# Performance work log

Measured on AMD Instinct MI355X. Metric: run time of the kernel, lower is better.

The kernel has to match this reference:

```python
import jax, jax.numpy as jnp
import numpy as np

B, S, H = 1, 2048, 2048
NH = 16            # num attention heads
QLR = 1536         # q_lora_rank
KVLR = 512         # kv_lora_rank
DR = 64            # qk_rope_head_dim
DN = 128           # qk_nope_head_dim
DV = 128           # v_head_dim
DQK = DN + DR      # qk_head_dim = 192
EPS = 1e-6


def rmsnorm(x, w):
    xf = x.astype(jnp.float32)
    var = jnp.mean(xf * xf, axis=-1, keepdims=True)
    return (xf * jax.lax.rsqrt(var + EPS)).astype(x.dtype) * w


def rotate_half(x):
    d = x.shape[-1] // 2
    return jnp.concatenate([-x[..., d:], x[..., :d]], axis=-1)


def rope_interleave(x, cos, sin):
    # x: [b, h, s, d]; de-interleave pairs (even dims -> first half, odd -> second)
    b, h, s, d = x.shape
    x = x.reshape(b, h, s, d // 2, 2).swapaxes(-1, -2).reshape(b, h, s, d)
    return x * cos + rotate_half(x) * sin


def setup_inputs() -> dict:
    key = jax.random.key(0)
    ks = jax.random.split(key, 8)
    std = 0.02
    hidden_states = jax.random.normal(ks[0], (B, S, H), jnp.float32)
    # real rotary cos/sin for a 64-dim rope slice
    pos = jnp.arange(S, dtype=jnp.float32)
    inv_freq = 1.0 / (10000.0 ** (jnp.arange(0, DR, 2, dtype=jnp.float32) / DR))
    ang = pos[:, None] * inv_freq[None, :]            # [S, DR//2]
    emb = jnp.concatenate([ang, ang], axis=-1)        # [S, DR]
    cos = jnp.broadcast_to(jnp.cos(emb)[None], (B, S, DR)).astype(jnp.float32)
    sin = jnp.broadcast_to(jnp.sin(emb)[None], (B, S, DR)).astype(jnp.float32)
    # weights stored [in, out]
    wq_a = jax.random.normal(ks[1], (H, QLR), jnp.float32) * std
    q_ln = jnp.ones((QLR,), jnp.float32)
    wq_b = jax.random.normal(ks[2], (QLR, NH * DQK), jnp.float32) * std
    wkv_a = jax.random.normal(ks[3], (H, KVLR + DR), jnp.float32) * std
    kv_ln = jnp.ones((KVLR,), jnp.float32)
    wkv_b = jax.random.normal(ks[4], (KVLR, NH * (DN + DV)), jnp.float32) * std
    wo = jax.random.normal(ks[5], (NH * DV, H), jnp.float32) * std
    return {"hidden_states": hidden_states, "cos": cos, "sin": sin,
            "wq_a": wq_a, "q_ln": q_ln, "wq_b": wq_b,
            "wkv_a": wkv_a, "kv_ln": kv_ln, "wkv_b": wkv_b, "wo": wo}


def reference(hidden_states, cos, sin, wq_a, q_ln, wq_b, wkv_a, kv_ln, wkv_b, wo):
    b, s, _ = hidden_states.shape
    # low-rank Q: a-proj -> RMSNorm -> b-proj
    q = rmsnorm(hidden_states @ wq_a, q_ln) @ wq_b           # [b, s, NH*DQK]
    q = q.reshape(b, s, NH, DQK).transpose(0, 2, 1, 3)       # [b, NH, s, DQK]
    q_pass, q_rot = q[..., :DN], q[..., DN:]
    # compressed KV with shared rope key
    ckv = hidden_states @ wkv_a                               # [b, s, KVLR+DR]
    kv_c, k_rot = ckv[..., :KVLR], ckv[..., KVLR:]
    kv = (rmsnorm(kv_c, kv_ln) @ wkv_b).reshape(b, s, NH, DN + DV).transpose(0, 2, 1, 3)
    k_pass, v = kv[..., :DN], kv[..., DN:]
    k_rot = k_rot[:, None, :, :]                              # [b, 1, s, DR]
    cos4, sin4 = cos[:, None], sin[:, None]
    q_rot = rope_interleave(q_rot, cos4, sin4)
    k_rot = rope_interleave(k_rot, cos4, sin4)
    k_rot = jnp.broadcast_to(k_rot, (b, NH, s, DR))
    qs = jnp.concatenate([q_pass, q_rot], axis=-1)            # [b, NH, s, DQK]
    ks_ = jnp.concatenate([k_pass, k_rot], axis=-1)
    scaling = DQK ** -0.5
    scores = jnp.einsum('bhqd,bhkd->bhqk', qs, ks_) * scaling
    causal = jnp.tril(jnp.ones((s, s), bool))
    scores = jnp.where(causal, scores, jnp.finfo(scores.dtype).min)
    probs = jax.nn.softmax(scores.astype(jnp.float32), axis=-1).astype(qs.dtype)
    out = jnp.einsum('bhqk,bhkd->bhqd', probs, v)             # [b, NH, s, DV]
    out = out.transpose(0, 2, 1, 3).reshape(b, s, NH * DV)
    return out @ wo
```

## Files before the change

kernel.cpp:

```cpp
#include <hip/hip_runtime.h>
#include <hip/hip_bf16.h>
#include <stdint.h>

#define S_    2048
#define H_    2048
#define NH_   16
#define QLR_  1536
#define KVLR_ 512
#define DR_   64
#define DN_   128
#define DV_   128
#define DQK_  192
#define QW_   (NH_*DQK_)
#define KVW_  (NH_*(DN_+DV_))
#define CKVW_ (KVLR_+DR_)

typedef __attribute__((ext_vector_type(8))) short short8;
typedef __attribute__((ext_vector_type(4))) float floatx4;

__device__ __forceinline__ unsigned short f2bf(float f) {
    unsigned u = __float_as_uint(f);
    unsigned r = u + 0x7fffu + ((u >> 16) & 1u);
    return (unsigned short)(r >> 16);
}
__device__ __forceinline__ float bf2f(unsigned short h) {
    return __uint_as_float(((unsigned)h) << 16);
}
__device__ __forceinline__ void store_out(float* p, float v) { *p = v; }
__device__ __forceinline__ void store_out(unsigned short* p, float v) { *p = f2bf(v); }

typedef const __attribute__((address_space(1))) unsigned int* gas_ptr;
typedef __attribute__((address_space(3))) unsigned int* las_ptr;
__device__ __forceinline__ void gload16(const void* g, void* l) {
    __builtin_amdgcn_global_load_lds((gas_ptr)g, (las_ptr)l, 16, 0, 0);
}

__device__ __forceinline__ int xcd_swz(int orig, int nwg) {
    int q8 = nwg >> 3, r8 = nwg & 7;
    int xcd = orig & 7, jj = orig >> 3;
    return (xcd < r8 ? xcd * (q8 + 1) : r8 * (q8 + 1) + (xcd - r8) * q8) + jj;
}

#define GEMM_STAGE(b, k0) do {                                               \
        _Pragma("unroll")                                                    \
        for (int sub = 0; sub < 2; ++sub) {                                  \
            int m = tid >> 2, k8 = tid & 3;                                  \
            gload16(A + (size_t)(bm + m) * lda + (k0) + sub * 32 + k8 * 8,   \
                    &As[b][sub][tid * 8]);                                   \
        }                                                                    \
        _Pragma("unroll")                                                    \
        for (int sub = 0; sub < 2; ++sub)                                    \
            _Pragma("unroll")                                                \
            for (int j = 0; j < 2; ++j) {                                    \
                int ch = j * 256 + tid;                                      \
                int n = ch >> 2, k8 = ch & 3;                                \
                int nrow = bn + n; if (nrow >= N) nrow = N - 1;              \
                gload16(Bt + (size_t)nrow * K + (k0) + sub * 32 + k8 * 8,    \
                        &Bs[b][sub][ch * 8]);                                \
            }                                                                \
    } while (0)

#define GEMM_COMPUTE_SUB(sub) do {                                           \
        short8 a[2], b[4];                                                   \
        _Pragma("unroll")                                                    \
        for (int mi = 0; mi < 2; ++mi)                                       \
            a[mi] = *(const short8*)&As[cur][sub][(wm + mi * 16 + cc) * 32 + g * 8]; \
        _Pragma("unroll")                                                    \
        for (int ni = 0; ni < 4; ++ni)                                       \
            b[ni] = *(const short8*)&Bs[cur][sub][(wn + ni * 16 + cc) * 32 + g * 8]; \
        __builtin_amdgcn_s_setprio(1);                                       \
        _Pragma("unroll")                                                    \
        for (int mi = 0; mi < 2; ++mi)                                       \
            _Pragma("unroll")                                                \
            for (int ni = 0; ni < 4; ++ni)                                   \
                acc[mi][ni] = __builtin_amdgcn_mfma_f32_16x16x32_bf16(       \
                    a[mi], b[ni], acc[mi][ni], 0, 0, 0);                     \
        __builtin_amdgcn_s_setprio(0);                                       \
    } while (0)

template <typename OutT>
__global__ __launch_bounds__(256) void gemm_bf16_db(
    const unsigned short* __restrict__ A, const unsigned short* __restrict__ Bt,
    OutT* __restrict__ C, int M, int N, int K, int lda, int ldc)
{
    __shared__ unsigned short As[2][2][64 * 32];
    __shared__ unsigned short Bs[2][2][128 * 32];

    const int tid = threadIdx.x;
    const int l = tid & 63;
    const int g = l >> 4, cc = l & 15;
    const int w = tid >> 6;
    const int wm = (w >> 1) * 32, wn = (w & 1) * 64;

    const int nwg = gridDim.x * gridDim.y;
    const int wg = xcd_swz(blockIdx.y * gridDim.x + blockIdx.x, nwg);
    const int bm = (wg / gridDim.x) * 64;
    const int bn = (wg % gridDim.x) * 128;

    floatx4 acc[2][4];
#pragma unroll
    for (int i = 0; i < 2; i++)
#pragma unroll
        for (int j = 0; j < 4; j++) acc[i][j] = (floatx4){0.f, 0.f, 0.f, 0.f};

    GEMM_STAGE(0, 0);
    __syncthreads();
    int cur = 0;

    for (int k0 = 0; k0 < K; k0 += 64) {
        if (k0 + 64 < K) GEMM_STAGE(cur ^ 1, k0 + 64);
        GEMM_COMPUTE_SUB(0);
        GEMM_COMPUTE_SUB(1);
        __syncthreads();
        cur ^= 1;
    }

#pragma unroll
    for (int mi = 0; mi < 2; ++mi)
#pragma unroll
        for (int ni = 0; ni < 4; ++ni)
#pragma unroll
            for (int i = 0; i < 4; ++i) {
                int row = bm + wm + mi * 16 + g * 4 + i;
                int col = bn + wn + ni * 16 + cc;
                if (col < N) store_out(&C[(size_t)row * ldc + col], acc[mi][ni][i]);
            }
}

__global__ __launch_bounds__(256) void gemm_bf16_dual(
    const unsigned short* __restrict__ A, const unsigned short* __restrict__ Bt,
    float* __restrict__ C0, float* __restrict__ C1,
    int M, int N, int K, int lda, int ldc0, int ldc1)
{
    __shared__ unsigned short As[2][2][64 * 32];
    __shared__ unsigned short Bs[2][2][128 * 32];

    const int tid = threadIdx.x;
    const int l = tid & 63;
    const int g = l >> 4, cc = l & 15;
    const int w = tid >> 6;
    const int wm = (w >> 1) * 32, wn = (w & 1) * 64;

    const int nwg = gridDim.x * gridDim.y;
    const int wg = xcd_swz(blockIdx.y * gridDim.x + blockIdx.x, nwg);
    const int bm = (wg / gridDim.x) * 64;
    const int bn = (wg % gridDim.x) * 128;

    floatx4 acc[2][4];
#pragma unroll
    for (int i = 0; i < 2; i++)
#pragma unroll
        for (int j = 0; j < 4; j++) acc[i][j] = (floatx4){0.f, 0.f, 0.f, 0.f};

    GEMM_STAGE(0, 0);
    __syncthreads();
    int cur = 0;

    for (int k0 = 0; k0 < K; k0 += 64) {
        if (k0 + 64 < K) GEMM_STAGE(cur ^ 1, k0 + 64);
        GEMM_COMPUTE_SUB(0);
        GEMM_COMPUTE_SUB(1);
        __syncthreads();
        cur ^= 1;
    }

#pragma unroll
    for (int mi = 0; mi < 2; ++mi)
#pragma unroll
        for (int ni = 0; ni < 4; ++ni)
#pragma unroll
            for (int i = 0; i < 4; ++i) {
                int row = bm + wm + mi * 16 + g * 4 + i;
                int col = bn + wn + ni * 16 + cc;
                if (col < QLR_)
                    C0[(size_t)row * ldc0 + col] = acc[mi][ni][i];
                else if (col < N)
                    C1[(size_t)row * ldc1 + (col - QLR_)] = acc[mi][ni][i];
            }
}

__global__ __launch_bounds__(256) void cast_bf16(
    const float* __restrict__ in, unsigned short* __restrict__ out, int n)
{
    int i = (blockIdx.x * 256 + threadIdx.x) * 4;
    if (i >= n) return;
    float4 v = *(const float4*)&in[i];
    ushort4 u;
    u.x = f2bf(v.x); u.y = f2bf(v.y); u.z = f2bf(v.z); u.w = f2bf(v.w);
    *(ushort4*)&out[i] = u;
}

__global__ __launch_bounds__(256) void transpose_cast(
    const float* __restrict__ W, unsigned short* __restrict__ Wt, int K, int N,
    float scl)
{
    __shared__ float t[32][33];
    const int n0 = blockIdx.x * 32, k0 = blockIdx.y * 32;
    const int tx = threadIdx.x & 31, ty4 = (threadIdx.x >> 5) * 4;
#pragma unroll
    for (int j = 0; j < 4; ++j)
        t[ty4 + j][tx] = W[(size_t)(k0 + ty4 + j) * N + n0 + tx];
    __syncthreads();
#pragma unroll
    for (int j = 0; j < 4; ++j)
        Wt[(size_t)(n0 + ty4 + j) * K + k0 + tx] = f2bf(t[tx][ty4 + j] * scl);
}

__global__ __launch_bounds__(256) void rmsnorm_bf16out(
    const float* __restrict__ x, const float* __restrict__ w,
    unsigned short* __restrict__ y, int cols, int xstride)
{
    const float* xr = x + (size_t)blockIdx.x * xstride;
    unsigned short* yr = y + (size_t)blockIdx.x * cols;
    const int tid = threadIdx.x;
    float ss = 0.f;
    for (int c = tid; c < cols; c += 256) { float v = xr[c]; ss += v * v; }
#pragma unroll
    for (int off = 32; off > 0; off >>= 1) ss += __shfl_xor(ss, off);
    __shared__ float red[4];
    if ((tid & 63) == 0) red[tid >> 6] = ss;
    __syncthreads();
    ss = red[0] + red[1] + red[2] + red[3];
    const float inv = rsqrtf(ss / (float)cols + 1e-6f);
    for (int c = tid; c < cols; c += 256) yr[c] = f2bf(xr[c] * inv * w[c]);
}

__global__ void rope_q_bf(unsigned short* __restrict__ q,
                          const float* __restrict__ cs, const float* __restrict__ sn)
{
    int t = blockIdx.x * 256 + threadIdx.x;
    int chunk = t >> 5, j = t & 31;
    int s = chunk >> 4, h = chunk & 15;
    unsigned short* x = q + (size_t)s * QW_ + h * DQK_ + DN_;
    float e = bf2f(x[2 * j]), o = bf2f(x[2 * j + 1]);
    float c = cs[s * DR_ + j], si = sn[s * DR_ + j];
    unsigned short u = f2bf(e * c - o * si);
    unsigned short v = f2bf(o * c + e * si);
    x[j] = u; x[j + 32] = v;
}

__global__ __launch_bounds__(256) void prep_k(
    const unsigned short* __restrict__ kvb, const float* __restrict__ ckv,
    const float* __restrict__ cs, const float* __restrict__ sn,
    unsigned short* __restrict__ kg)
{
    const int s = blockIdx.x, tid = threadIdx.x;
    __shared__ unsigned short rot[64];
    if (tid < 32) {
        int j = tid;
        const float* x = ckv + (size_t)s * CKVW_ + KVLR_;
        float e = x[2 * j], o = x[2 * j + 1];
        float c = cs[s * DR_ + j], si = sn[s * DR_ + j];
        rot[j] = f2bf(e * c - o * si);
        rot[j + 32] = f2bf(o * c + e * si);
    }
    __syncthreads();
    const int sw = s & 7;
    for (int ch = tid; ch < 384; ch += 256) {
        int hh = ch / 24, d8 = ch % 24;
        short8 v;
        if (d8 < 16)
            v = *(const short8*)&kvb[(size_t)s * KVW_ + hh * 256 + d8 * 8];
        else
            v = *(const short8*)&rot[(d8 - 16) * 8];
        int d8s = d8 ^ sw;
        *(short8*)&kg[((size_t)hh * S_ + s) * 192 + d8s * 8] = v;
    }
}

__global__ __launch_bounds__(256) void transpose_v(
    const unsigned short* __restrict__ kvb, unsigned short* __restrict__ vt)
{
    __shared__ unsigned short t[32][36];
    const int dv0 = blockIdx.x * 32, s0 = blockIdx.y * 32, h = blockIdx.z;
    const int r = threadIdx.x >> 3, c4 = threadIdx.x & 7;
    ushort4 ld = *(const ushort4*)&kvb[(size_t)(s0 + r) * KVW_ + h * 256 + 128 + dv0 + c4 * 4];
    t[r][c4 * 4 + 0] = ld.x; t[r][c4 * 4 + 1] = ld.y;
    t[r][c4 * 4 + 2] = ld.z; t[r][c4 * 4 + 3] = ld.w;
    __syncthreads();
    ushort4 st;
    st.x = t[c4 * 4 + 0][r]; st.y = t[c4 * 4 + 1][r];
    st.z = t[c4 * 4 + 2][r]; st.w = t[c4 * 4 + 3][r];
    *(ushort4*)&vt[(size_t)(h * 128 + dv0 + r) * S_ + s0 + c4 * 4] = st;
}

__global__ __launch_bounds__(256, 3) void flash_attn7(
    const unsigned short* __restrict__ qg, const unsigned short* __restrict__ kg,
    const unsigned short* __restrict__ vt,
    unsigned short* __restrict__ op0, unsigned short* __restrict__ op1,
    float* __restrict__ mlp)
{
    const int bid = blockIdx.x;
    const int qblk = 31 - (bid >> 5);
    const int low5 = bid & 31;
    const int h = low5 & 15;
    const int sp = low5 >> 4;
    const int pb = h * 32 + qblk;

    __shared__ unsigned short sm[2 * 6144 + 2 * 4096 + 4 * 640];
    unsigned short* Kb = sm;
    unsigned short* Vb = sm + 12288;
    const int tid = threadIdx.x;
    const int w = tid >> 6;
    const int l = tid & 63, g = l >> 4, cc = l & 15;
    unsigned short* Pw = sm + 20480 + w * 640;

    const int qmin = qblk * 64 + w * 16;
    const int q_lane = qmin + cc;
    const int wave_qmax = qmin + 15;
    const int HT = qblk + 1;
    const int kt_begin = sp * HT, kt_end = kt_begin + HT;

    const unsigned short* kh = kg + (size_t)h * S_ * 192;
    const unsigned short* vh = vt + (size_t)(h * 128) * S_;

    short8 qf[6];
    {
        const unsigned short* qb = qg + (size_t)q_lane * QW_ + h * DQK_;
#pragma unroll
        for (int k6 = 0; k6 < 6; ++k6)
            qf[k6] = *(const short8*)&qb[k6 * 32 + g * 8];
    }

    floatx4 accO[8];
#pragma unroll
    for (int nt = 0; nt < 8; ++nt) accO[nt] = (floatx4){0.f, 0.f, 0.f, 0.f};
    float m_r = -1e30f, l_r = 0.f;

#define STAGE_KV(b, kt) do {                                             \
        const unsigned short* ksrc = kh + (size_t)(kt) * 32 * 192;       \
        _Pragma("unroll")                                                \
        for (int j = 0; j < 3; ++j) {                                    \
            int ch = j * 256 + tid;                                      \
            gload16(ksrc + ch * 8, Kb + (b) * 6144 + ch * 8);            \
        }                                                                \
        const int krow = (kt) * 32;                                      \
        _Pragma("unroll")                                                \
        for (int j = 0; j < 2; ++j) {                                    \
            int ch = j * 256 + tid;                                      \
            int dv = ch >> 2, j8 = ch & 3;                               \
            gload16(vh + (size_t)dv * S_ + krow + j8 * 8,                \
                    Vb + (b) * 4096 + ch * 8);                           \
        }                                                                \
    } while (0)

    STAGE_KV(0, kt_begin);
    int cur = 0;

    for (int kt = kt_begin; kt < kt_end; ++kt) {
        const int krow0 = kt * 32;
        __syncthreads();
        if (kt + 1 < kt_end) STAGE_KV(cur ^ 1, kt + 1);

        if (krow0 <= wave_qmax) {
            const unsigned short* Kc = Kb + cur * 6144;
            const unsigned short* Vc = Vb + cur * 4096;
            const int swz = (cc & 7) << 3;

            floatx4 s0 = (floatx4){0.f, 0.f, 0.f, 0.f};
            floatx4 s1 = (floatx4){0.f, 0.f, 0.f, 0.f};
            __builtin_amdgcn_s_setprio(1);
#pragma unroll
            for (int k6 = 0; k6 < 6; ++k6) {
                short8 b0 = *(const short8*)&Kc[cc * 192 + ((k6 * 32 + g * 8) ^ swz)];
                short8 b1 = *(const short8*)&Kc[(16 + cc) * 192 + ((k6 * 32 + g * 8) ^ swz)];
                s0 = __builtin_amdgcn_mfma_f32_16x16x32_bf16(b0, qf[k6], s0, 0, 0, 0);
                s1 = __builtin_amdgcn_mfma_f32_16x16x32_bf16(b1, qf[k6], s1, 0, 0, 0);
            }
            __builtin_amdgcn_s_setprio(0);

            float v0[4], v1[4];
            if (krow0 + 31 <= qmin) {
#pragma unroll
                for (int i = 0; i < 4; ++i) { v0[i] = s0[i]; v1[i] = s1[i]; }
            } else {
#pragma unroll
                for (int i = 0; i < 4; ++i) {
                    v0[i] = (krow0 + g * 4 + i) <= q_lane ? s0[i] : -1e30f;
                    v1[i] = (krow0 + 16 + g * 4 + i) <= q_lane ? s1[i] : -1e30f;
                }
            }
            float mt = fmaxf(fmaxf(fmaxf(v0[0], v0[1]), fmaxf(v0[2], v0[3])),
                             fmaxf(fmaxf(v1[0], v1[1]), fmaxf(v1[2], v1[3])));
            mt = fmaxf(mt, __shfl_xor(mt, 16));
            mt = fmaxf(mt, __shfl_xor(mt, 32));

            if (!__all(mt <= m_r + 6.0f)) {
                float mn = fmaxf(m_r, mt);
                float alpha = exp2f(m_r - mn);
                m_r = mn;
                l_r *= alpha;
                float aB[4];
#pragma unroll
                for (int i = 0; i < 4; ++i) aB[i] = __shfl(alpha, g * 4 + i);
#pragma unroll
                for (int nt = 0; nt < 8; ++nt)
#pragma unroll
                    for (int i = 0; i < 4; ++i) accO[nt][i] *= aB[i];
            }

            float p0[4], p1[4], ps = 0.f;
#pragma unroll
            for (int i = 0; i < 4; ++i) {
                p0[i] = exp2f(v0[i] - m_r);
                p1[i] = exp2f(v1[i] - m_r);
                ps += p0[i] + p1[i];
            }
            ps += __shfl_xor(ps, 16);
            ps += __shfl_xor(ps, 32);
            l_r += ps;

            {
                ushort4 u0, u1;
                u0.x = f2bf(p0[0]); u0.y = f2bf(p0[1]);
                u0.z = f2bf(p0[2]); u0.w = f2bf(p0[3]);
                u1.x = f2bf(p1[0]); u1.y = f2bf(p1[1]);
                u1.z = f2bf(p1[2]); u1.w = f2bf(p1[3]);
                *(ushort4*)&Pw[cc * 40 + g * 4] = u0;
                *(ushort4*)&Pw[cc * 40 + 16 + g * 4] = u1;
            }

            short8 pf = *(const short8*)&Pw[cc * 40 + g * 8];
            __builtin_amdgcn_s_setprio(1);
#pragma unroll
            for (int nt = 0; nt < 8; ++nt) {
                short8 vr = *(const short8*)&Vc[(nt * 16 + cc) * 32 + g * 8];
                accO[nt] = __builtin_amdgcn_mfma_f32_16x16x32_bf16(pf, vr, accO[nt], 0, 0, 0);
            }
            __builtin_amdgcn_s_setprio(0);
        }
        cur ^= 1;
    }
#undef STAGE_KV

    float mB[4], lB[4];
#pragma unroll
    for (int i = 0; i < 4; ++i) {
        int src = (g << 4) | (g * 4 + i);
        mB[i] = __shfl(m_r, src);
        lB[i] = __shfl(l_r, src);
    }
    unsigned short* op = sp ? op1 : op0;
#pragma unroll
    for (int nt = 0; nt < 8; ++nt)
#pragma unroll
        for (int i = 0; i < 4; ++i)
            op[(size_t)pb * 8192 + (w * 16 + g * 4 + i) * 128 + nt * 16 + cc] =
                f2bf(accO[nt][i]);
    if (cc == 0) {
#pragma unroll
        for (int i = 0; i < 4; ++i) {
            size_t mi = ((size_t)(sp * 512 + pb) * 64 + w * 16 + g * 4 + i) * 2;
            mlp[mi + 0] = mB[i];
            mlp[mi + 1] = lB[i];
        }
    }
}

__global__ __launch_bounds__(256) void merge_attn(
    const unsigned short* __restrict__ op0, const unsigned short* __restrict__ op1,
    const float* __restrict__ mlp, unsigned short* __restrict__ ao)
{
    const int pb = blockIdx.x;
    const int h = pb >> 5, qblk = pb & 31;
    const int tid = threadIdx.x;
    const int row = tid >> 2, c0 = (tid & 3) * 32;

    const size_t mi0 = ((size_t)pb * 64 + row) * 2;
    const size_t mi1 = ((size_t)(512 + pb) * 64 + row) * 2;
    float m0 = mlp[mi0 + 0], l0 = mlp[mi0 + 1];
    float m1 = mlp[mi1 + 0], l1 = mlp[mi1 + 1];
    float mf = fmaxf(m0, m1);
    float e0 = exp2f(m0 - mf), e1 = exp2f(m1 - mf);
    float inv = 1.f / (l0 * e0 + l1 * e1);
    float w0 = e0 * inv, w1 = e1 * inv;

    const size_t pbase = (size_t)pb * 8192 + row * 128 + c0;
    unsigned short* dst = ao + (size_t)(qblk * 64 + row) * (NH_ * DV_) + h * DV_ + c0;
#pragma unroll
    for (int j = 0; j < 4; ++j) {
        short8 a = *(const short8*)&op0[pbase + j * 8];
        short8 b = *(const short8*)&op1[pbase + j * 8];
        short8 o;
#pragma unroll
        for (int k = 0; k < 8; ++k)
            o[k] = (short)f2bf(bf2f((unsigned short)a[k]) * w0 +
                               bf2f((unsigned short)b[k]) * w1);
        *(short8*)&dst[j * 8] = o;
    }
}

extern "C" void kernel_launch(void* const* d_in, const int* in_sizes, int n_in,
                              void* d_out, int out_size, void* d_ws, size_t ws_size,
                              hipStream_t stream)
{
    const float* hs    = (const float*)d_in[0];
    const float* cosp  = (const float*)d_in[1];
    const float* sinp  = (const float*)d_in[2];
    const float* wq_a  = (const float*)d_in[3];
    const float* q_ln  = (const float*)d_in[4];
    const float* wq_b  = (const float*)d_in[5];
    const float* wkv_a = (const float*)d_in[6];
    const float* kv_ln = (const float*)d_in[7];
    const float* wkv_b = (const float*)d_in[8];
    const float* wo    = (const float*)d_in[9];
    float* out = (float*)d_out;

    char* ws = (char*)d_ws;
    float*          qa     = (float*)(ws);
    float*          ckv    = (float*)(ws + 12582912);
    unsigned short* q_bf   = (unsigned short*)(ws + 17301504);
    unsigned short* kvb    = (unsigned short*)(ws + 29884416);
    unsigned short* hs_bf  = (unsigned short*)(ws + 46661632);
    unsigned short* qa_bf  = (unsigned short*)(ws + 55050240);
    unsigned short* ckv_bf = (unsigned short*)(ws + 61341696);
    unsigned short* ao_bf  = (unsigned short*)(ws + 63438848);
    unsigned short* wt     = (unsigned short*)(ws + 71827456);
    unsigned short* kg     = (unsigned short*)qa;
    unsigned short* vtb    = hs_bf;

    unsigned short* op0 = qa_bf;
    unsigned short* op1 = wt;
    float*          mlp = ckv;

    const float qscale = 0.07216878364870322f * 1.4426950408889634f;

    cast_bf16<<<(S_ * H_) / 1024, 256, 0, stream>>>(hs, hs_bf, S_ * H_);

    transpose_cast<<<dim3(QLR_ / 32, H_ / 32), 256, 0, stream>>>(wq_a, wt, H_, QLR_, 1.f);
    transpose_cast<<<dim3(CKVW_ / 32, H_ / 32), 256, 0, stream>>>(
        wkv_a, wt + (size_t)QLR_ * H_, H_, CKVW_, 1.f);
    gemm_bf16_dual<<<dim3((QLR_ + CKVW_ + 127) / 128, S_ / 64), 256, 0, stream>>>(
        hs_bf, wt, qa, ckv, S_, QLR_ + CKVW_, H_, H_, QLR_, CKVW_);
    rmsnorm_bf16out<<<S_, 256, 0, stream>>>(qa, q_ln, qa_bf, QLR_, QLR_);
    rmsnorm_bf16out<<<S_, 256, 0, stream>>>(ckv, kv_ln, ckv_bf, KVLR_, CKVW_);

    transpose_cast<<<dim3(QW_ / 32, QLR_ / 32), 256, 0, stream>>>(wq_b, wt, QLR_, QW_, qscale);
    gemm_bf16_db<unsigned short><<<dim3(QW_ / 128, S_ / 64), 256, 0, stream>>>(
        qa_bf, wt, q_bf, S_, QW_, QLR_, QLR_, QW_);
    rope_q_bf<<<(S_ * NH_ * 32) / 256, 256, 0, stream>>>(q_bf, cosp, sinp);

    transpose_cast<<<dim3(KVW_ / 32, KVLR_ / 32), 256, 0, stream>>>(wkv_b, wt, KVLR_, KVW_, 1.f);
    gemm_bf16_db<unsigned short><<<dim3(KVW_ / 128, S_ / 64), 256, 0, stream>>>(
        ckv_bf, wt, kvb, S_, KVW_, KVLR_, KVLR_, KVW_);

    prep_k<<<S_, 256, 0, stream>>>(kvb, ckv, cosp, sinp, kg);
    transpose_v<<<dim3(4, 64, 16), 256, 0, stream>>>(kvb, vtb);

    flash_attn7<<<1024, 256, 0, stream>>>(q_bf, kg, vtb, op0, op1, mlp);
    merge_attn<<<512, 256, 0, stream>>>(op0, op1, mlp, ao_bf);

    transpose_cast<<<dim3(H_ / 32, H_ / 32), 256, 0, stream>>>(wo, wt, H_, H_, 1.f);
    gemm_bf16_db<float><<<dim3(H_ / 128, S_ / 64), 256, 0, stream>>>(
        ao_bf, wt, out, S_, H_, NH_ * DV_, NH_ * DV_, H_);
}
```

Measured before the change: 222.1 us.

## Use 128-row query blocks with 8 waves and 4-way KV split in attention

The flash-attention kernel now uses 512-thread blocks covering 128 query rows, so each staged K/V tile is shared by eight waves instead of four. The KV range is split four ways instead of two, which keeps the grid at 1024 blocks. The merge kernel now combines four partial outputs using the per-split max and sum statistics. This cuts redundant K/V loads per query, at the cost of more partial-output traffic, a heavier merge and extra workspace buffers that reuse the kvb region.

```diff
diff --git a/kernel.cpp b/kernel.cpp
--- a/kernel.cpp
+++ b/kernel.cpp
@@ -284,20 +284,21 @@
     *(ushort4*)&vt[(size_t)(h * 128 + dv0 + r) * S_ + s0 + c4 * 4] = st;
 }
 
-__global__ __launch_bounds__(256, 3) void flash_attn7(
+__global__ __launch_bounds__(512, 4) void flash_attn8(
     const unsigned short* __restrict__ qg, const unsigned short* __restrict__ kg,
     const unsigned short* __restrict__ vt,
     unsigned short* __restrict__ op0, unsigned short* __restrict__ op1,
+    unsigned short* __restrict__ op2, unsigned short* __restrict__ op3,
     float* __restrict__ mlp)
 {
     const int bid = blockIdx.x;
-    const int qblk = 31 - (bid >> 5);
-    const int low5 = bid & 31;
-    const int h = low5 & 15;
-    const int sp = low5 >> 4;
-    const int pb = h * 32 + qblk;
-
-    __shared__ unsigned short sm[2 * 6144 + 2 * 4096 + 4 * 640];
+    const int j = 15 - (bid >> 6);
+    const int low6 = bid & 63;
+    const int h = low6 & 15;
+    const int sp = low6 >> 4;
+    const int pb = h * 16 + j;
+
+    __shared__ unsigned short sm[2 * 6144 + 2 * 4096 + 8 * 640];
     unsigned short* Kb = sm;
     unsigned short* Vb = sm + 12288;
     const int tid = threadIdx.x;
@@ -305,11 +306,11 @@
     const int l = tid & 63, g = l >> 4, cc = l & 15;
     unsigned short* Pw = sm + 20480 + w * 640;
 
-    const int qmin = qblk * 64 + w * 16;
+    const int qmin = j * 128 + w * 16;
     const int q_lane = qmin + cc;
     const int wave_qmax = qmin + 15;
-    const int HT = qblk + 1;
-    const int kt_begin = sp * HT, kt_end = kt_begin + HT;
+    const int cnt = j + 1;
+    const int kt_begin = sp * cnt, kt_end = kt_begin + cnt;
 
     const unsigned short* kh = kg + (size_t)h * S_ * 192;
     const unsigned short* vh = vt + (size_t)(h * 128) * S_;
@@ -329,18 +330,15 @@
 
 #define STAGE_KV(b, kt) do {                                             \
         const unsigned short* ksrc = kh + (size_t)(kt) * 32 * 192;       \
-        _Pragma("unroll")                                                \
-        for (int j = 0; j < 3; ++j) {                                    \
-            int ch = j * 256 + tid;                                      \
-            gload16(ksrc + ch * 8, Kb + (b) * 6144 + ch * 8);            \
-        }                                                                \
+        gload16(ksrc + tid * 8, Kb + (b) * 6144 + tid * 8);              \
+        if (tid < 256)                                                   \
+            gload16(ksrc + (512 + tid) * 8,                              \
+                    Kb + (b) * 6144 + (512 + tid) * 8);                  \
         const int krow = (kt) * 32;                                      \
-        _Pragma("unroll")                                                \
-        for (int j = 0; j < 2; ++j) {                                    \
-            int ch = j * 256 + tid;                                      \
-            int dv = ch >> 2, j8 = ch & 3;                               \
+        {                                                                \
+            int dv = tid >> 2, j8 = tid & 3;                             \
             gload16(vh + (size_t)dv * S_ + krow + j8 * 8,                \
-                    Vb + (b) * 4096 + ch * 8);                           \
+                    Vb + (b) * 4096 + tid * 8);                          \
         }                                                                \
     } while (0)
 
@@ -440,53 +438,63 @@
         mB[i] = __shfl(m_r, src);
         lB[i] = __shfl(l_r, src);
     }
-    unsigned short* op = sp ? op1 : op0;
+    unsigned short* op = (sp == 0) ? op0 : (sp == 1) ? op1 : (sp == 2) ? op2 : op3;
 #pragma unroll
     for (int nt = 0; nt < 8; ++nt)
 #pragma unroll
         for (int i = 0; i < 4; ++i)
-            op[(size_t)pb * 8192 + (w * 16 + g * 4 + i) * 128 + nt * 16 + cc] =
+            op[(size_t)pb * 16384 + (w * 16 + g * 4 + i) * 128 + nt * 16 + cc] =
                 f2bf(accO[nt][i]);
     if (cc == 0) {
 #pragma unroll
         for (int i = 0; i < 4; ++i) {
-            size_t mi = ((size_t)(sp * 512 + pb) * 64 + w * 16 + g * 4 + i) * 2;
+            size_t mi = ((size_t)(sp * 256 + pb) * 128 + w * 16 + g * 4 + i) * 2;
             mlp[mi + 0] = mB[i];
             mlp[mi + 1] = lB[i];
         }
     }
 }
 
-__global__ __launch_bounds__(256) void merge_attn(
+__global__ __launch_bounds__(256) void merge_attn4(
     const unsigned short* __restrict__ op0, const unsigned short* __restrict__ op1,
+    const unsigned short* __restrict__ op2, const unsigned short* __restrict__ op3,
     const float* __restrict__ mlp, unsigned short* __restrict__ ao)
 {
     const int pb = blockIdx.x;
-    const int h = pb >> 5, qblk = pb & 31;
+    const int h = pb >> 4, j = pb & 15;
     const int tid = threadIdx.x;
-    const int row = tid >> 2, c0 = (tid & 3) * 32;
-
-    const size_t mi0 = ((size_t)pb * 64 + row) * 2;
-    const size_t mi1 = ((size_t)(512 + pb) * 64 + row) * 2;
-    float m0 = mlp[mi0 + 0], l0 = mlp[mi0 + 1];
-    float m1 = mlp[mi1 + 0], l1 = mlp[mi1 + 1];
-    float mf = fmaxf(m0, m1);
-    float e0 = exp2f(m0 - mf), e1 = exp2f(m1 - mf);
-    float inv = 1.f / (l0 * e0 + l1 * e1);
-    float w0 = e0 * inv, w1 = e1 * inv;
-
-    const size_t pbase = (size_t)pb * 8192 + row * 128 + c0;
-    unsigned short* dst = ao + (size_t)(qblk * 64 + row) * (NH_ * DV_) + h * DV_ + c0;
-#pragma unroll
-    for (int j = 0; j < 4; ++j) {
-        short8 a = *(const short8*)&op0[pbase + j * 8];
-        short8 b = *(const short8*)&op1[pbase + j * 8];
+    const int row = tid >> 1, c0 = (tid & 1) * 64;
+
+    float m[4], lv[4];
+#pragma unroll
+    for (int i = 0; i < 4; ++i) {
+        size_t mi = ((size_t)(i * 256 + pb) * 128 + row) * 2;
+        m[i] = mlp[mi + 0];
+        lv[i] = mlp[mi + 1];
+    }
+    float mf = fmaxf(fmaxf(m[0], m[1]), fmaxf(m[2], m[3]));
+    float e[4], lsum = 0.f;
+#pragma unroll
+    for (int i = 0; i < 4; ++i) { e[i] = exp2f(m[i] - mf); lsum += lv[i] * e[i]; }
+    float inv = 1.f / lsum;
+    float w0 = e[0] * inv, w1 = e[1] * inv, w2 = e[2] * inv, w3 = e[3] * inv;
+
+    const size_t pbase = (size_t)pb * 16384 + row * 128 + c0;
+    unsigned short* dst = ao + (size_t)(j * 128 + row) * (NH_ * DV_) + h * DV_ + c0;
+#pragma unroll
+    for (int seg = 0; seg < 8; ++seg) {
+        short8 a0 = *(const short8*)&op0[pbase + seg * 8];
+        short8 a1 = *(const short8*)&op1[pbase + seg * 8];
+        short8 a2 = *(const short8*)&op2[pbase + seg * 8];
+        short8 a3 = *(const short8*)&op3[pbase + seg * 8];
         short8 o;
 #pragma unroll
         for (int k = 0; k < 8; ++k)
-            o[k] = (short)f2bf(bf2f((unsigned short)a[k]) * w0 +
-                               bf2f((unsigned short)b[k]) * w1);
-        *(short8*)&dst[j * 8] = o;
+            o[k] = (short)f2bf(bf2f((unsigned short)a0[k]) * w0 +
+                               bf2f((unsigned short)a1[k]) * w1 +
+                               bf2f((unsigned short)a2[k]) * w2 +
+                               bf2f((unsigned short)a3[k]) * w3);
+        *(short8*)&dst[seg * 8] = o;
     }
 }
 
@@ -521,6 +529,8 @@
 
     unsigned short* op0 = qa_bf;
     unsigned short* op1 = wt;
+    unsigned short* op2 = kvb;
+    unsigned short* op3 = kvb + 4194304;
     float*          mlp = ckv;
 
     const float qscale = 0.07216878364870322f * 1.4426950408889634f;
@@ -547,8 +557,8 @@
     prep_k<<<S_, 256, 0, stream>>>(kvb, ckv, cosp, sinp, kg);
     transpose_v<<<dim3(4, 64, 16), 256, 0, stream>>>(kvb, vtb);
 
-    flash_attn7<<<1024, 256, 0, stream>>>(q_bf, kg, vtb, op0, op1, mlp);
-    merge_attn<<<512, 256, 0, stream>>>(op0, op1, mlp, ao_bf);
+    flash_attn8<<<1024, 512, 0, stream>>>(q_bf, kg, vtb, op0, op1, op2, op3, mlp);
+    merge_attn4<<<256, 256, 0, stream>>>(op0, op1, op2, op3, mlp, ao_bf);
 
     transpose_cast<<<dim3(H_ / 32, H_ / 32), 256, 0, stream>>>(wo, wt, H_, H_, 1.f);
     gemm_bf16_db<float><<<dim3(H_ / 128, S_ / 64), 256, 0, stream>>>(
```

Measured after the change: 242.1 us. 1.09x slower.
